# Optimization experiments

Measured on AMD Instinct MI355X. Metric: run time of the kernel, lower is better.

The kernel has to match this reference:

```python
import jax, jax.numpy as jnp
import numpy as np

B, N, M = 2, 4096, 4096
DQ = DKV = DOUT = 512
HEADS, DH = 8, 64
INNER = HEADS * DH
SCALE = DH ** -0.5


def _ln(x, g, b, eps=1e-5):
    mu = jnp.mean(x, axis=-1, keepdims=True)
    var = jnp.mean(jnp.square(x - mu), axis=-1, keepdims=True)
    return (x - mu) * jax.lax.rsqrt(var + eps) * g + b


def setup_inputs() -> dict:
    key = jax.random.key(0)
    ks = jax.random.split(key, 12)
    s = lambda fan: 1.0 / np.sqrt(fan)
    return {
        "q0": jax.random.normal(ks[0], (B, N, DQ), jnp.float32),
        "kv0": jax.random.normal(ks[1], (B, M, DKV), jnp.float32),
        "normq_g": jnp.ones((DQ,), jnp.float32),
        "normq_b": jnp.zeros((DQ,), jnp.float32),
        "normkv_g": jnp.ones((DKV,), jnp.float32),
        "normkv_b": jnp.zeros((DKV,), jnp.float32),
        "Wq": jax.random.normal(ks[2], (DQ, INNER), jnp.float32) * s(DQ),
        "Wk": jax.random.normal(ks[3], (DKV, INNER), jnp.float32) * s(DKV),
        "Wv": jax.random.normal(ks[4], (DKV, INNER), jnp.float32) * s(DKV),
        "Wr": jax.random.normal(ks[5], (INNER, DQ), jnp.float32) * s(INNER),
        "mlp_g": jnp.ones((DQ,), jnp.float32),
        "mlp_b": jnp.zeros((DQ,), jnp.float32),
        "W1": jax.random.normal(ks[6], (DQ, DOUT), jnp.float32) * s(DQ),
        "b1": jnp.zeros((DOUT,), jnp.float32),
        "W2": jax.random.normal(ks[7], (DOUT, DOUT), jnp.float32) * s(DOUT),
        "b2": jnp.zeros((DOUT,), jnp.float32),
    }


def reference(q0, kv0, normq_g, normq_b, normkv_g, normkv_b,
              Wq, Wk, Wv, Wr, mlp_g, mlp_b, W1, b1, W2, b2):
    # projections
    q = _ln(q0, normq_g, normq_b) @ Wq                    # [B,N,INNER]
    kv = _ln(kv0, normkv_g, normkv_b)                     # [B,M,DKV]
    k = kv @ Wk                                           # [B,M,INNER]
    v = kv @ Wv                                           # [B,M,INNER]
    # split heads: b n (h d) -> b h n d
    q = q.reshape(B, N, HEADS, DH).transpose(0, 2, 1, 3)
    k = k.reshape(B, M, HEADS, DH).transpose(0, 2, 1, 3)
    v = v.reshape(B, M, HEADS, DH).transpose(0, 2, 1, 3)
    dots = jnp.einsum('bhnd,bhmd->bhnm', q, k) * SCALE    # [B,H,N,M]
    attn = jax.nn.softmax(dots, axis=-1)
    out = jnp.einsum('bhnm,bhmd->bhnd', attn, v)          # [B,H,N,DH]
    out = out.transpose(0, 2, 1, 3).reshape(B, N, INNER)  # b h n d -> b n (h d)
    out = out @ Wr + q0                                   # [B,N,DQ]
    # MLP branch with residual
    h = _ln(out, mlp_g, mlp_b)
    h = jax.nn.relu(h @ W1 + b1) @ W2 + b2
    return out + h
```

## Files before the change

### kernel.cpp

```cpp
#include <hip/hip_runtime.h>

typedef unsigned short u16;
typedef unsigned int u32;
typedef __bf16 bf16x8 __attribute__((ext_vector_type(8)));
typedef float f32x4 __attribute__((ext_vector_type(4)));
typedef u16 u16x8 __attribute__((ext_vector_type(8)));

#define SC2 0.18033688011112042f

__device__ __forceinline__ u16 bf16rne(float f) {
  u32 u = __float_as_uint(f);
  u32 r = (u + 0x7FFFu + ((u >> 16) & 1u)) >> 16;
  return (u16)r;
}
__device__ __forceinline__ u32 packrne(float a, float b) {
  return (u32)bf16rne(a) | ((u32)bf16rne(b) << 16);
}
__device__ __forceinline__ float b2f(u16 v) {
  return __uint_as_float(((u32)v) << 16);
}

__device__ __forceinline__ void async16(const void* g, void* l) {
  __builtin_amdgcn_global_load_lds(
      (__attribute__((address_space(1))) void*)(g),
      (__attribute__((address_space(3))) void*)(l), 16, 0, 0);
}
template <int N>
__device__ __forceinline__ void vm_wait() {
  asm volatile("s_waitcnt vmcnt(%0)" ::"n"(N) : "memory");
}
__device__ __forceinline__ void lgkm_wait0() {
  asm volatile("s_waitcnt lgkmcnt(0)" ::: "memory");
}
__device__ __forceinline__ void bar() {
  asm volatile("s_barrier" ::: "memory");
}

__device__ __forceinline__ void ln_row(const float* xr, const float* gp,
                                       const float* bp, u16* orow, int lane) {
  const float* xl = xr + lane * 8;
  float4 a0 = *(const float4*)xl;
  float4 a1 = *(const float4*)(xl + 4);
  float v[8] = {a0.x, a0.y, a0.z, a0.w, a1.x, a1.y, a1.z, a1.w};
  float s = 0.f, s2 = 0.f;
#pragma unroll
  for (int j = 0; j < 8; ++j) { s += v[j]; s2 += v[j] * v[j]; }
#pragma unroll
  for (int off = 32; off; off >>= 1) {
    s += __shfl_xor(s, off);
    s2 += __shfl_xor(s2, off);
  }
  float mu = s * (1.0f / 512.0f);
  float rstd = rsqrtf(s2 * (1.0f / 512.0f) - mu * mu + 1e-5f);
  const float* gl = gp + lane * 8;
  const float* bl = bp + lane * 8;
  float4 g0 = *(const float4*)gl, g1 = *(const float4*)(gl + 4);
  float4 b0 = *(const float4*)bl, b1 = *(const float4*)(bl + 4);
  float gg[8] = {g0.x, g0.y, g0.z, g0.w, g1.x, g1.y, g1.z, g1.w};
  float bb[8] = {b0.x, b0.y, b0.z, b0.w, b1.x, b1.y, b1.z, b1.w};
  u16x8 ov;
#pragma unroll
  for (int j = 0; j < 8; ++j) ov[j] = bf16rne((v[j] - mu) * rstd * gg[j] + bb[j]);
  *(u16x8*)(orow + lane * 8) = ov;
}

__device__ __forceinline__ void lnb_row(const u16* xr, const float* gp,
                                        const float* bp, u16* orow, int lane) {
  u16x8 xv = *(const u16x8*)(xr + lane * 8);
  float v[8];
#pragma unroll
  for (int j = 0; j < 8; ++j) v[j] = b2f(xv[j]);
  float s = 0.f, s2 = 0.f;
#pragma unroll
  for (int j = 0; j < 8; ++j) { s += v[j]; s2 += v[j] * v[j]; }
#pragma unroll
  for (int off = 32; off; off >>= 1) {
    s += __shfl_xor(s, off);
    s2 += __shfl_xor(s2, off);
  }
  float mu = s * (1.0f / 512.0f);
  float rstd = rsqrtf(s2 * (1.0f / 512.0f) - mu * mu + 1e-5f);
  const float* gl = gp + lane * 8;
  const float* bl = bp + lane * 8;
  float4 g0 = *(const float4*)gl, g1 = *(const float4*)(gl + 4);
  float4 b0 = *(const float4*)bl, b1 = *(const float4*)(bl + 4);
  float gg[8] = {g0.x, g0.y, g0.z, g0.w, g1.x, g1.y, g1.z, g1.w};
  float bb[8] = {b0.x, b0.y, b0.z, b0.w, b1.x, b1.y, b1.z, b1.w};
  u16x8 ov;
#pragma unroll
  for (int j = 0; j < 8; ++j) ov[j] = bf16rne((v[j] - mu) * rstd * gg[j] + bb[j]);
  *(u16x8*)(orow + lane * 8) = ov;
}

__global__ __launch_bounds__(256) void prep_kernel(
    const float* __restrict__ w0, const float* __restrict__ w1,
    const float* __restrict__ w2, const float* __restrict__ w3,
    const float* __restrict__ w4, const float* __restrict__ w5,
    u16* __restrict__ wout,
    const float* __restrict__ x0, const float* __restrict__ g0,
    const float* __restrict__ b0, u16* __restrict__ o0,
    const float* __restrict__ x1, const float* __restrict__ g1,
    const float* __restrict__ b1, u16* __restrict__ o1) {
  __shared__ u16 T[64 * 72];
  int t = threadIdx.x;
  int bx = blockIdx.x;
  if (bx < 384) {
    int widx = bx >> 6, tile = bx & 63;
    int k0 = (tile & 7) * 64, n0 = (tile >> 3) * 64;
    const float* W = w0;
    if (widx == 1) W = w1; else if (widx == 2) W = w2; else if (widx == 3) W = w3;
    else if (widx == 4) W = w4; else if (widx == 5) W = w5;
#pragma unroll
    for (int p = 0; p < 4; ++p) {
      int kr = p * 16 + (t >> 4);
      int nc = (t & 15) * 4;
      float4 v = *(const float4*)(W + (size_t)(k0 + kr) * 512 + n0 + nc);
      T[(nc + 0) * 72 + kr] = bf16rne(v.x);
      T[(nc + 1) * 72 + kr] = bf16rne(v.y);
      T[(nc + 2) * 72 + kr] = bf16rne(v.z);
      T[(nc + 3) * 72 + kr] = bf16rne(v.w);
    }
    __syncthreads();
    u16* ob = wout + (size_t)widx * 262144;
#pragma unroll
    for (int p = 0; p < 2; ++p) {
      int idx = p * 256 + t;
      int nr = idx >> 3, ch = idx & 7;
      uint4 val = *(const uint4*)(T + nr * 72 + ch * 8);
      *(uint4*)(ob + (size_t)(n0 + nr) * 512 + k0 + ch * 8) = val;
    }
  } else {
    int w = t >> 6, lane = t & 63;
    size_t row = (size_t)(bx - 384) * 4 + w;
    if (row < 8192) {
      ln_row(x0 + row * 512, g0, b0, o0 + row * 512, lane);
    } else {
      size_t r2 = row - 8192;
      ln_row(x1 + r2 * 512, g1, b1, o1 + r2 * 512, lane);
    }
  }
}

__global__ __launch_bounds__(256) void lnb_kernel(
    const u16* __restrict__ x, const float* __restrict__ g,
    const float* __restrict__ b, u16* __restrict__ o) {
  int w = threadIdx.x >> 6, lane = threadIdx.x & 63;
  size_t row = (size_t)blockIdx.x * 4 + w;
  lnb_row(x + row * 512, g, b, o + row * 512, lane);
}

#define GSTAGE(buf, k0)                                                          \
  {                                                                              \
    _Pragma("unroll") for (int i = 0; i < 2; ++i) {                              \
      int s = t + 256 * i;                                                       \
      int mts = s >> 6, L = s & 63;                                             \
      async16(A + (size_t)(row0 + mts * 16 + (L & 15)) * 512 + (k0) + (L >> 4) * 8, \
              (char*)As[buf] + s * 16);                                          \
    }                                                                            \
    {                                                                            \
      int s = t;                                                                 \
      int nts = s >> 6, L = s & 63;                                             \
      async16(Bt + (size_t)(col0 + nts * 16 + (L & 15)) * 512 + (k0) + (L >> 4) * 8, \
              (char*)Bs[buf] + s * 16);                                          \
    }                                                                            \
  }

#define GEMM_CORE                                                                \
  GSTAGE(0, 0);                                                                  \
  GSTAGE(1, 32);                                                                 \
  GSTAGE(2, 64);                                                                 \
  _Pragma("unroll") for (int kk = 0; kk < 16; ++kk) {                            \
    if (kk <= 13) vm_wait<6>();                                                  \
    else if (kk == 14) vm_wait<3>();                                             \
    else vm_wait<0>();                                                           \
    bar();                                                                       \
    if (kk < 13) GSTAGE((kk + 3) & 3, (kk + 3) * 32);                            \
    const u16* Ac = As[kk & 3];                                                  \
    const u16* Bc = Bs[kk & 3];                                                  \
    bf16x8 Af[2], Bf[4];                                                         \
    _Pragma("unroll") for (int mt = 0; mt < 2; ++mt)                             \
        Af[mt] = *(const bf16x8*)(Ac + ((w * 2 + mt) * 64 + lane) * 8);          \
    _Pragma("unroll") for (int nt = 0; nt < 4; ++nt)                             \
        Bf[nt] = *(const bf16x8*)(Bc + (nt * 64 + lane) * 8);                    \
    _Pragma("unroll") for (int mt = 0; mt < 2; ++mt)                             \
        _Pragma("unroll") for (int nt = 0; nt < 4; ++nt)                         \
            acc[mt][nt] = __builtin_amdgcn_mfma_f32_16x16x32_bf16(               \
                Af[mt], Bf[nt], acc[mt][nt], 0, 0, 0);                           \
  }

template <int MODE>
__global__ __launch_bounds__(256) void gemm512_kernel(
    const u16* __restrict__ A, const u16* __restrict__ Bt, void* __restrict__ Cv,
    const float* __restrict__ bias, const float* __restrict__ res) {
  __shared__ __align__(16) u16 As[4][4096];
  __shared__ __align__(16) u16 Bs[4][2048];
  const int t = threadIdx.x;
  const int lane = t & 63;
  const int w = t >> 6;
  const int row0 = blockIdx.x * 128;
  const int col0 = blockIdx.y * 64;
  f32x4 acc[2][4];
#pragma unroll
  for (int i = 0; i < 2; ++i)
#pragma unroll
    for (int j = 0; j < 4; ++j) acc[i][j] = (f32x4){0.f, 0.f, 0.f, 0.f};

  GEMM_CORE

  const int q = lane >> 4, cl = lane & 15;
#pragma unroll
  for (int mt = 0; mt < 2; ++mt) {
#pragma unroll
    for (int nt = 0; nt < 4; ++nt) {
      int col = col0 + nt * 16 + cl;
#pragma unroll
      for (int r = 0; r < 4; ++r) {
        int row = row0 + (w * 2 + mt) * 16 + q * 4 + r;
        float v = acc[mt][nt][r];
        size_t idx = (size_t)row * 512 + col;
        if (MODE == 2) {
          v += bias[col];
          ((u16*)Cv)[idx] = bf16rne(fmaxf(v, 0.f));
        } else if (MODE == 3) {
          ((float*)Cv)[idx] = v + bias[col] + b2f(((const u16*)res)[idx]);
        } else if (MODE == 7) {
          ((u16*)Cv)[idx] = bf16rne(v + res[idx]);
        }
      }
    }
  }
}

__global__ __launch_bounds__(256) void proj_kernel(
    const u16* __restrict__ Aq, const u16* __restrict__ BtQ, u16* __restrict__ Qp,
    const u16* __restrict__ Akv, const u16* __restrict__ BtKV,
    u16* __restrict__ Kp, u16* __restrict__ VTp) {
  __shared__ __align__(16) u16 As[4][4096];
  __shared__ __align__(16) u16 Bs[4][2048];
  const int t = threadIdx.x;
  const int lane = t & 63;
  const int w = t >> 6;
  const int by = blockIdx.y;
  const bool isq = by < 8;
  const u16* A = isq ? Aq : Akv;
  const u16* Bt = isq ? BtQ : BtKV;
  const int row0 = blockIdx.x * 128;
  const int col0 = (isq ? by : by - 8) * 64;
  f32x4 acc[2][4];
#pragma unroll
  for (int i = 0; i < 2; ++i)
#pragma unroll
    for (int j = 0; j < 4; ++j) acc[i][j] = (f32x4){0.f, 0.f, 0.f, 0.f};

  GEMM_CORE

  const int q = lane >> 4, cl = lane & 15;
#pragma unroll
  for (int mt = 0; mt < 2; ++mt) {
#pragma unroll
    for (int nt = 0; nt < 4; ++nt) {
      int col = col0 + nt * 16 + cl;
      if (!isq && col >= 512) {
        int d = col - 512;
        int bb = row0 >> 12;
        int mloc = (row0 & 4095) + (w * 2 + mt) * 16 + q * 4;
        uint2 pk;
        pk.x = packrne(acc[mt][nt][0], acc[mt][nt][1]);
        pk.y = packrne(acc[mt][nt][2], acc[mt][nt][3]);
        *(uint2*)(VTp + ((size_t)bb * 512 + d) * 4096 + mloc) = pk;
        continue;
      }
#pragma unroll
      for (int r = 0; r < 4; ++r) {
        int row = row0 + (w * 2 + mt) * 16 + q * 4 + r;
        float v = acc[mt][nt][r];
        if (isq) {
          Qp[(size_t)row * 512 + col] = bf16rne(v * SC2);
        } else {
          Kp[(size_t)row * 512 + col] = bf16rne(v);
        }
      }
    }
  }
}

__global__ __launch_bounds__(128, 2) void attn_kernel(
    const u16* __restrict__ Q, const u16* __restrict__ K,
    const u16* __restrict__ VT, u16* __restrict__ O0, u16* __restrict__ O1,
    float* __restrict__ lpart) {
  __shared__ __align__(16) u16 Ks[2][4096];
  __shared__ __align__(16) u16 Vs[2][4096];
  __shared__ __align__(16) u16 Ps[2][1024];
  const int t = threadIdx.x;
  const int lane = t & 63;
  const int w = t >> 6;
  const int g = lane >> 4, cl = lane & 15;
  const int h = blockIdx.x, qt = blockIdx.y;
  const int b = blockIdx.z >> 1, sp = blockIdx.z & 1;
  const u16* Qg = Q + ((size_t)(b * 4096 + qt * 128 + w * 64)) * 512 + h * 64;
  const u16* Kg = K + ((size_t)(b * 4096 + sp * 2048)) * 512 + h * 64;
  const u16* VTg = VT + ((size_t)(b * 512 + h * 64)) * 4096 + sp * 2048;
  u16* Ob = (sp ? O1 : O0) + (((size_t)(b * 8 + h) * 4096) + qt * 128 + w * 64) * 64;
  float* lb = lpart + ((size_t)((sp * 2 + b) * 8 + h)) * 4096 + qt * 128 + w * 64;
  char* Pw = (char*)Ps[w];

#pragma unroll
  for (int i = 0; i < 8; ++i) {
    async16(Qg + (size_t)((i >> 1) * 16 + cl) * 512 + (i & 1) * 32 + g * 8,
            (char*)Ks[w] + (i * 64 + lane) * 16);
  }
  vm_wait<0>();
  bf16x8 Qb[4][2];
#pragma unroll
  for (int nt = 0; nt < 4; ++nt)
#pragma unroll
    for (int ks = 0; ks < 2; ++ks)
      Qb[nt][ks] = *(const bf16x8*)((char*)Ks[w] + ((nt * 2 + ks) * 64 + lane) * 16);
  lgkm_wait0();
  bar();

#define STAGEKV(buf, m0)                                                          \
  {                                                                               \
    _Pragma("unroll") for (int i = 0; i < 4; ++i) {                               \
      int s = t + 128 * i; int c = s >> 6; int L = s & 63;                        \
      async16(Kg + (size_t)((m0) + (c >> 1) * 16 + (L & 15)) * 512 + (c & 1) * 32 + (L >> 4) * 8, \
              (char*)Ks[buf] + s * 16);                                           \
    }                                                                             \
    _Pragma("unroll") for (int i = 0; i < 4; ++i) {                               \
      int s = t + 128 * i; int c = s >> 6; int L = s & 63;                        \
      async16(VTg + (size_t)((c >> 1) * 16 + (L & 15)) * 4096 + (m0) + (c & 1) * 32 + (L >> 4) * 8, \
              (char*)Vs[buf] + s * 16);                                           \
    }                                                                             \
  }

  STAGEKV(0, 0);

  u16x8 ou;
#pragma unroll
  for (int j = 0; j < 8; ++j) ou[j] = 0x3F80;
  bf16x8 ones = __builtin_bit_cast(bf16x8, ou);

  f32x4 Oa[4][4], ls[4];
#pragma unroll
  for (int i = 0; i < 4; ++i) {
    ls[i] = (f32x4){0.f, 0.f, 0.f, 0.f};
#pragma unroll
    for (int j = 0; j < 4; ++j) Oa[i][j] = (f32x4){0.f, 0.f, 0.f, 0.f};
  }
  const int s7 = cl & 7;

  for (int it = 0; it < 32; ++it) {
    if (it < 31) {
      STAGEKV((it + 1) & 1, (it + 1) * 64);
      vm_wait<8>();
    } else {
      vm_wait<0>();
    }
    bar();
    const u16* Kc = Ks[it & 1];
    const u16* Vc = Vs[it & 1];
    bf16x8 Kf[4][2], Vf[4][2];
#pragma unroll
    for (int mt = 0; mt < 4; ++mt)
#pragma unroll
      for (int ks = 0; ks < 2; ++ks) {
        Kf[mt][ks] = *(const bf16x8*)((const char*)Kc + ((mt * 2 + ks) * 64 + lane) * 16);
        Vf[mt][ks] = *(const bf16x8*)((const char*)Vc + ((mt * 2 + ks) * 64 + lane) * 16);
      }

#pragma unroll
    for (int nt = 0; nt < 4; ++nt) {
      f32x4 St[4];
#pragma unroll
      for (int mt = 0; mt < 4; ++mt) St[mt] = (f32x4){0.f, 0.f, 0.f, 0.f};
#pragma unroll
      for (int ks = 0; ks < 2; ++ks)
#pragma unroll
        for (int mt = 0; mt < 4; ++mt)
          St[mt] = __builtin_amdgcn_mfma_f32_16x16x32_bf16(Kf[mt][ks], Qb[nt][ks], St[mt], 0, 0, 0);

#pragma unroll
      for (int mt = 0; mt < 4; ++mt) {
        float p0 = __builtin_amdgcn_exp2f(St[mt][0]);
        float p1 = __builtin_amdgcn_exp2f(St[mt][1]);
        float p2 = __builtin_amdgcn_exp2f(St[mt][2]);
        float p3 = __builtin_amdgcn_exp2f(St[mt][3]);
        uint2 pk;
        pk.x = __builtin_amdgcn_perm(__float_as_uint(p1), __float_as_uint(p0), 0x07060302u);
        pk.y = __builtin_amdgcn_perm(__float_as_uint(p3), __float_as_uint(p2), 0x07060302u);
        *(uint2*)(Pw + cl * 128 + (((mt * 2 + (g >> 1)) ^ s7) << 4) + ((g & 1) << 3)) = pk;
      }
      bf16x8 Pb[2];
#pragma unroll
      for (int ks = 0; ks < 2; ++ks)
        Pb[ks] = *(const bf16x8*)(Pw + cl * 128 + (((ks * 4 + g) ^ s7) << 4));
      ls[nt] = __builtin_amdgcn_mfma_f32_16x16x32_bf16(ones, Pb[0], ls[nt], 0, 0, 0);
      ls[nt] = __builtin_amdgcn_mfma_f32_16x16x32_bf16(ones, Pb[1], ls[nt], 0, 0, 0);
#pragma unroll
      for (int ks = 0; ks < 2; ++ks)
#pragma unroll
        for (int mtd = 0; mtd < 4; ++mtd)
          Oa[mtd][nt] = __builtin_amdgcn_mfma_f32_16x16x32_bf16(Vf[mtd][ks], Pb[ks], Oa[mtd][nt], 0, 0, 0);
    }
    bar();
  }

#pragma unroll
  for (int nt = 0; nt < 4; ++nt) {
    int q = nt * 16 + cl;
#pragma unroll
    for (int mtd = 0; mtd < 4; ++mtd) {
      uint2 pk;
      pk.x = packrne(Oa[mtd][nt][0], Oa[mtd][nt][1]);
      pk.y = packrne(Oa[mtd][nt][2], Oa[mtd][nt][3]);
      *(uint2*)(Ob + (size_t)q * 64 + mtd * 16 + g * 4) = pk;
    }
    if (g == 0) lb[q] = ls[nt][0];
  }
}

__global__ __launch_bounds__(256) void combine_kernel(
    const u16* __restrict__ O0, const u16* __restrict__ O1,
    const float* __restrict__ lp, u16* __restrict__ out) {
  int idx = blockIdx.x * 256 + threadIdx.x;
  int dc = idx & 7;
  int q = (idx >> 3) & 4095;
  int h = (idx >> 15) & 7;
  int b = idx >> 18;
  size_t po = (((size_t)(b * 8 + h) * 4096) + q) * 64 + dc * 8;
  u16x8 a = *(const u16x8*)(O0 + po);
  u16x8 c = *(const u16x8*)(O1 + po);
  float l0 = lp[((size_t)(b * 8 + h)) * 4096 + q];
  float l1 = lp[((size_t)(16 + b * 8 + h)) * 4096 + q];
  float inv = 1.0f / (l0 + l1);
  u16x8 o;
#pragma unroll
  for (int j = 0; j < 8; ++j) o[j] = bf16rne((b2f(a[j]) + b2f(c[j])) * inv);
  *(u16x8*)(out + ((size_t)(b * 4096 + q)) * 512 + h * 64 + dc * 8) = o;
}

extern "C" void kernel_launch(void* const* d_in, const int* in_sizes, int n_in,
                              void* d_out, int out_size, void* d_ws, size_t ws_size,
                              hipStream_t stream) {
  const float* q0 = (const float*)d_in[0];
  const float* kv0 = (const float*)d_in[1];
  const float* nq_g = (const float*)d_in[2];
  const float* nq_b = (const float*)d_in[3];
  const float* nkv_g = (const float*)d_in[4];
  const float* nkv_b = (const float*)d_in[5];
  const float* Wq = (const float*)d_in[6];
  const float* Wk = (const float*)d_in[7];
  const float* Wv = (const float*)d_in[8];
  const float* Wr = (const float*)d_in[9];
  const float* mlp_g = (const float*)d_in[10];
  const float* mlp_b = (const float*)d_in[11];
  const float* W1 = (const float*)d_in[12];
  const float* b1 = (const float*)d_in[13];
  const float* W2 = (const float*)d_in[14];
  const float* b2 = (const float*)d_in[15];
  float* out = (float*)d_out;

  char* ws = (char*)d_ws;
  u16* obb = (u16*)(ws + 0);
  u16* O1p = (u16*)(ws + 0);
  u16* Qp = (u16*)(ws + 16777216);
  u16* aout = (u16*)(ws + 16777216);
  u16* Kp = (u16*)(ws + 25165824);
  u16* h1 = (u16*)(ws + 25165824);
  u16* VTp = (u16*)(ws + 33554432);
  u16* kvn2 = (u16*)(ws + 33554432);
  u16* wb = (u16*)(ws + 41943040);
  float* lpart = (float*)(ws + 45088768);
  u16* qn = (u16*)(ws + 46137344);
  u16* O0p = (u16*)(ws + 46137344);
  u16* kvn = (u16*)(ws + 54525952);
  u16* wqT = wb;
  u16* wkT = wb + 262144;
  u16* wrT = wb + 786432;
  u16* w1T = wb + 1048576;
  u16* w2T = wb + 1310720;

  dim3 blk(256);
  prep_kernel<<<4480, blk, 0, stream>>>(Wq, Wk, Wv, Wr, W1, W2, wb,
                                        q0, nq_g, nq_b, qn, kv0, nkv_g, nkv_b, kvn);
  proj_kernel<<<dim3(64, 24), blk, 0, stream>>>(qn, wqT, Qp, kvn, wkT, Kp, VTp);
  attn_kernel<<<dim3(8, 32, 4), dim3(128), 0, stream>>>(Qp, Kp, VTp, O0p, O1p, lpart);
  combine_kernel<<<2048, blk, 0, stream>>>(O0p, O1p, lpart, aout);
  gemm512_kernel<7><<<dim3(64, 8), blk, 0, stream>>>(aout, wrT, obb, nullptr, q0);
  lnb_kernel<<<2048, blk, 0, stream>>>(obb, mlp_g, mlp_b, kvn2);
  gemm512_kernel<2><<<dim3(64, 8), blk, 0, stream>>>(kvn2, w1T, h1, b1, nullptr);
  gemm512_kernel<3><<<dim3(64, 8), blk, 0, stream>>>(h1, w2T, out, b2, (const float*)obb);
}
```

Measured before the change: 286.4 us.

## Halve GEMM row tiles and split attention keys four ways for more blocks

All 512-wide GEMMs and the projection kernel now use 64-row tiles, so their grids have twice as many blocks. The attention kernel splits the key dimension into four chunks instead of two and processes 32-key tiles with smaller LDS buffers. It also raises its occupancy hint to 3 blocks per SM. The combine kernel now sums four partial outputs and four partial row sums. The aim is to fill the MI355X's many CUs better. The cost is more partial-output traffic, a heavier combine pass, and less data reuse per tile.

```diff
diff --git a/kernel.cpp b/kernel.cpp
--- a/kernel.cpp
+++ b/kernel.cpp
@@ -149,83 +149,71 @@
   lnb_row(x + row * 512, g, b, o + row * 512, lane);
 }
 
-#define GSTAGE(buf, k0)                                                          \
+#define GSTAGE64(buf, k0)                                                        \
   {                                                                              \
-    _Pragma("unroll") for (int i = 0; i < 2; ++i) {                              \
-      int s = t + 256 * i;                                                       \
-      int mts = s >> 6, L = s & 63;                                             \
-      async16(A + (size_t)(row0 + mts * 16 + (L & 15)) * 512 + (k0) + (L >> 4) * 8, \
-              (char*)As[buf] + s * 16);                                          \
+    {                                                                            \
+      int c = t >> 6, L = t & 63;                                                \
+      async16(A + (size_t)(row0 + c * 16 + (L & 15)) * 512 + (k0) + (L >> 4) * 8,\
+              (char*)As[buf] + t * 16);                                          \
+      async16(Bt + (size_t)(col0 + c * 16 + (L & 15)) * 512 + (k0) + (L >> 4) * 8,\
+              (char*)Bs[buf] + t * 16);                                          \
     }                                                                            \
-    {                                                                            \
-      int s = t;                                                                 \
-      int nts = s >> 6, L = s & 63;                                             \
-      async16(Bt + (size_t)(col0 + nts * 16 + (L & 15)) * 512 + (k0) + (L >> 4) * 8, \
-              (char*)Bs[buf] + s * 16);                                          \
-    }                                                                            \
-  }
-
-#define GEMM_CORE                                                                \
-  GSTAGE(0, 0);                                                                  \
-  GSTAGE(1, 32);                                                                 \
-  GSTAGE(2, 64);                                                                 \
+  }
+
+#define GEMM64_CORE                                                              \
+  GSTAGE64(0, 0);                                                                \
+  GSTAGE64(1, 32);                                                               \
+  GSTAGE64(2, 64);                                                               \
   _Pragma("unroll") for (int kk = 0; kk < 16; ++kk) {                            \
-    if (kk <= 13) vm_wait<6>();                                                  \
-    else if (kk == 14) vm_wait<3>();                                             \
+    if (kk <= 13) vm_wait<4>();                                                  \
+    else if (kk == 14) vm_wait<2>();                                             \
     else vm_wait<0>();                                                           \
     bar();                                                                       \
-    if (kk < 13) GSTAGE((kk + 3) & 3, (kk + 3) * 32);                            \
+    if (kk < 13) GSTAGE64((kk + 3) & 3, (kk + 3) * 32);                          \
     const u16* Ac = As[kk & 3];                                                  \
     const u16* Bc = Bs[kk & 3];                                                  \
-    bf16x8 Af[2], Bf[4];                                                         \
-    _Pragma("unroll") for (int mt = 0; mt < 2; ++mt)                             \
-        Af[mt] = *(const bf16x8*)(Ac + ((w * 2 + mt) * 64 + lane) * 8);          \
+    bf16x8 Af = *(const bf16x8*)(Ac + (w * 64 + lane) * 8);                      \
+    bf16x8 Bf[4];                                                                \
     _Pragma("unroll") for (int nt = 0; nt < 4; ++nt)                             \
         Bf[nt] = *(const bf16x8*)(Bc + (nt * 64 + lane) * 8);                    \
-    _Pragma("unroll") for (int mt = 0; mt < 2; ++mt)                             \
-        _Pragma("unroll") for (int nt = 0; nt < 4; ++nt)                         \
-            acc[mt][nt] = __builtin_amdgcn_mfma_f32_16x16x32_bf16(               \
-                Af[mt], Bf[nt], acc[mt][nt], 0, 0, 0);                           \
+    _Pragma("unroll") for (int nt = 0; nt < 4; ++nt)                             \
+        acc[nt] = __builtin_amdgcn_mfma_f32_16x16x32_bf16(Af, Bf[nt], acc[nt],   \
+                                                          0, 0, 0);              \
   }
 
 template <int MODE>
 __global__ __launch_bounds__(256) void gemm512_kernel(
     const u16* __restrict__ A, const u16* __restrict__ Bt, void* __restrict__ Cv,
     const float* __restrict__ bias, const float* __restrict__ res) {
-  __shared__ __align__(16) u16 As[4][4096];
+  __shared__ __align__(16) u16 As[4][2048];
   __shared__ __align__(16) u16 Bs[4][2048];
   const int t = threadIdx.x;
   const int lane = t & 63;
   const int w = t >> 6;
-  const int row0 = blockIdx.x * 128;
+  const int row0 = blockIdx.x * 64;
   const int col0 = blockIdx.y * 64;
-  f32x4 acc[2][4];
-#pragma unroll
-  for (int i = 0; i < 2; ++i)
-#pragma unroll
-    for (int j = 0; j < 4; ++j) acc[i][j] = (f32x4){0.f, 0.f, 0.f, 0.f};
-
-  GEMM_CORE
-
-  const int q = lane >> 4, cl = lane & 15;
-#pragma unroll
-  for (int mt = 0; mt < 2; ++mt) {
-#pragma unroll
-    for (int nt = 0; nt < 4; ++nt) {
-      int col = col0 + nt * 16 + cl;
-#pragma unroll
-      for (int r = 0; r < 4; ++r) {
-        int row = row0 + (w * 2 + mt) * 16 + q * 4 + r;
-        float v = acc[mt][nt][r];
-        size_t idx = (size_t)row * 512 + col;
-        if (MODE == 2) {
-          v += bias[col];
-          ((u16*)Cv)[idx] = bf16rne(fmaxf(v, 0.f));
-        } else if (MODE == 3) {
-          ((float*)Cv)[idx] = v + bias[col] + b2f(((const u16*)res)[idx]);
-        } else if (MODE == 7) {
-          ((u16*)Cv)[idx] = bf16rne(v + res[idx]);
-        }
+  f32x4 acc[4];
+#pragma unroll
+  for (int j = 0; j < 4; ++j) acc[j] = (f32x4){0.f, 0.f, 0.f, 0.f};
+
+  GEMM64_CORE
+
+  const int g = lane >> 4, cl = lane & 15;
+#pragma unroll
+  for (int nt = 0; nt < 4; ++nt) {
+    int col = col0 + nt * 16 + cl;
+#pragma unroll
+    for (int r = 0; r < 4; ++r) {
+      int row = row0 + w * 16 + g * 4 + r;
+      float v = acc[nt][r];
+      size_t idx = (size_t)row * 512 + col;
+      if (MODE == 2) {
+        v += bias[col];
+        ((u16*)Cv)[idx] = bf16rne(fmaxf(v, 0.f));
+      } else if (MODE == 3) {
+        ((float*)Cv)[idx] = v + bias[col] + b2f(((const u16*)res)[idx]);
+      } else if (MODE == 7) {
+        ((u16*)Cv)[idx] = bf16rne(v + res[idx]);
       }
     }
   }
@@ -235,7 +223,7 @@
     const u16* __restrict__ Aq, const u16* __restrict__ BtQ, u16* __restrict__ Qp,
     const u16* __restrict__ Akv, const u16* __restrict__ BtKV,
     u16* __restrict__ Kp, u16* __restrict__ VTp) {
-  __shared__ __align__(16) u16 As[4][4096];
+  __shared__ __align__(16) u16 As[4][2048];
   __shared__ __align__(16) u16 Bs[4][2048];
   const int t = threadIdx.x;
   const int lane = t & 63;
@@ -244,70 +232,67 @@
   const bool isq = by < 8;
   const u16* A = isq ? Aq : Akv;
   const u16* Bt = isq ? BtQ : BtKV;
-  const int row0 = blockIdx.x * 128;
+  const int row0 = blockIdx.x * 64;
   const int col0 = (isq ? by : by - 8) * 64;
-  f32x4 acc[2][4];
-#pragma unroll
-  for (int i = 0; i < 2; ++i)
-#pragma unroll
-    for (int j = 0; j < 4; ++j) acc[i][j] = (f32x4){0.f, 0.f, 0.f, 0.f};
-
-  GEMM_CORE
-
-  const int q = lane >> 4, cl = lane & 15;
-#pragma unroll
-  for (int mt = 0; mt < 2; ++mt) {
-#pragma unroll
-    for (int nt = 0; nt < 4; ++nt) {
-      int col = col0 + nt * 16 + cl;
-      if (!isq && col >= 512) {
-        int d = col - 512;
-        int bb = row0 >> 12;
-        int mloc = (row0 & 4095) + (w * 2 + mt) * 16 + q * 4;
-        uint2 pk;
-        pk.x = packrne(acc[mt][nt][0], acc[mt][nt][1]);
-        pk.y = packrne(acc[mt][nt][2], acc[mt][nt][3]);
-        *(uint2*)(VTp + ((size_t)bb * 512 + d) * 4096 + mloc) = pk;
-        continue;
+  f32x4 acc[4];
+#pragma unroll
+  for (int j = 0; j < 4; ++j) acc[j] = (f32x4){0.f, 0.f, 0.f, 0.f};
+
+  GEMM64_CORE
+
+  const int g = lane >> 4, cl = lane & 15;
+#pragma unroll
+  for (int nt = 0; nt < 4; ++nt) {
+    int col = col0 + nt * 16 + cl;
+    if (!isq && col >= 512) {
+      int d = col - 512;
+      int bb = row0 >> 12;
+      int mloc = (row0 & 4095) + w * 16 + g * 4;
+      uint2 pk;
+      pk.x = packrne(acc[nt][0], acc[nt][1]);
+      pk.y = packrne(acc[nt][2], acc[nt][3]);
+      *(uint2*)(VTp + ((size_t)bb * 512 + d) * 4096 + mloc) = pk;
+      continue;
+    }
+#pragma unroll
+    for (int r = 0; r < 4; ++r) {
+      int row = row0 + w * 16 + g * 4 + r;
+      float v = acc[nt][r];
+      if (isq) {
+        Qp[(size_t)row * 512 + col] = bf16rne(v * SC2);
+      } else {
+        Kp[(size_t)row * 512 + col] = bf16rne(v);
       }
-#pragma unroll
-      for (int r = 0; r < 4; ++r) {
-        int row = row0 + (w * 2 + mt) * 16 + q * 4 + r;
-        float v = acc[mt][nt][r];
-        if (isq) {
-          Qp[(size_t)row * 512 + col] = bf16rne(v * SC2);
-        } else {
-          Kp[(size_t)row * 512 + col] = bf16rne(v);
-        }
-      }
-    }
-  }
-}
-
-__global__ __launch_bounds__(128, 2) void attn_kernel(
+    }
+  }
+}
+
+__global__ __launch_bounds__(128, 3) void attn_kernel(
     const u16* __restrict__ Q, const u16* __restrict__ K,
     const u16* __restrict__ VT, u16* __restrict__ O0, u16* __restrict__ O1,
-    float* __restrict__ lpart) {
-  __shared__ __align__(16) u16 Ks[2][4096];
-  __shared__ __align__(16) u16 Vs[2][4096];
-  __shared__ __align__(16) u16 Ps[2][1024];
+    u16* __restrict__ O2, u16* __restrict__ O3, float* __restrict__ lpart) {
+  __shared__ __align__(16) u16 Ks[2][2048];
+  __shared__ __align__(16) u16 Vs[2][2048];
+  __shared__ __align__(16) u16 Ps[2][512];
   const int t = threadIdx.x;
   const int lane = t & 63;
   const int w = t >> 6;
   const int g = lane >> 4, cl = lane & 15;
   const int h = blockIdx.x, qt = blockIdx.y;
-  const int b = blockIdx.z >> 1, sp = blockIdx.z & 1;
+  const int b = blockIdx.z >> 2, sp = blockIdx.z & 3;
   const u16* Qg = Q + ((size_t)(b * 4096 + qt * 128 + w * 64)) * 512 + h * 64;
-  const u16* Kg = K + ((size_t)(b * 4096 + sp * 2048)) * 512 + h * 64;
-  const u16* VTg = VT + ((size_t)(b * 512 + h * 64)) * 4096 + sp * 2048;
-  u16* Ob = (sp ? O1 : O0) + (((size_t)(b * 8 + h) * 4096) + qt * 128 + w * 64) * 64;
+  const u16* Kg = K + ((size_t)(b * 4096 + sp * 1024)) * 512 + h * 64;
+  const u16* VTg = VT + ((size_t)(b * 512 + h * 64)) * 4096 + sp * 1024;
+  u16* Op = (sp == 0) ? O0 : (sp == 1) ? O1 : (sp == 2) ? O2 : O3;
+  u16* Ob = Op + (((size_t)(b * 8 + h) * 4096) + qt * 128 + w * 64) * 64;
   float* lb = lpart + ((size_t)((sp * 2 + b) * 8 + h)) * 4096 + qt * 128 + w * 64;
   char* Pw = (char*)Ps[w];
+  char* Qscr = w ? (char*)Vs : (char*)Ks;
 
 #pragma unroll
   for (int i = 0; i < 8; ++i) {
     async16(Qg + (size_t)((i >> 1) * 16 + cl) * 512 + (i & 1) * 32 + g * 8,
-            (char*)Ks[w] + (i * 64 + lane) * 16);
+            Qscr + (i * 64 + lane) * 16);
   }
   vm_wait<0>();
   bf16x8 Qb[4][2];
@@ -315,20 +300,20 @@
   for (int nt = 0; nt < 4; ++nt)
 #pragma unroll
     for (int ks = 0; ks < 2; ++ks)
-      Qb[nt][ks] = *(const bf16x8*)((char*)Ks[w] + ((nt * 2 + ks) * 64 + lane) * 16);
+      Qb[nt][ks] = *(const bf16x8*)(Qscr + ((nt * 2 + ks) * 64 + lane) * 16);
   lgkm_wait0();
   bar();
 
 #define STAGEKV(buf, m0)                                                          \
   {                                                                               \
-    _Pragma("unroll") for (int i = 0; i < 4; ++i) {                               \
+    _Pragma("unroll") for (int i = 0; i < 2; ++i) {                               \
       int s = t + 128 * i; int c = s >> 6; int L = s & 63;                        \
       async16(Kg + (size_t)((m0) + (c >> 1) * 16 + (L & 15)) * 512 + (c & 1) * 32 + (L >> 4) * 8, \
               (char*)Ks[buf] + s * 16);                                           \
     }                                                                             \
-    _Pragma("unroll") for (int i = 0; i < 4; ++i) {                               \
+    _Pragma("unroll") for (int i = 0; i < 2; ++i) {                               \
       int s = t + 128 * i; int c = s >> 6; int L = s & 63;                        \
-      async16(VTg + (size_t)((c >> 1) * 16 + (L & 15)) * 4096 + (m0) + (c & 1) * 32 + (L >> 4) * 8, \
+      async16(VTg + (size_t)(c * 16 + (L & 15)) * 4096 + (m0) + (L >> 4) * 8,     \
               (char*)Vs[buf] + s * 16);                                           \
     }                                                                             \
   }
@@ -347,40 +332,41 @@
 #pragma unroll
     for (int j = 0; j < 4; ++j) Oa[i][j] = (f32x4){0.f, 0.f, 0.f, 0.f};
   }
-  const int s7 = cl & 7;
+  const int s3 = cl & 3;
 
   for (int it = 0; it < 32; ++it) {
     if (it < 31) {
-      STAGEKV((it + 1) & 1, (it + 1) * 64);
-      vm_wait<8>();
+      STAGEKV((it + 1) & 1, (it + 1) * 32);
+      vm_wait<4>();
     } else {
       vm_wait<0>();
     }
     bar();
     const u16* Kc = Ks[it & 1];
     const u16* Vc = Vs[it & 1];
-    bf16x8 Kf[4][2], Vf[4][2];
-#pragma unroll
-    for (int mt = 0; mt < 4; ++mt)
-#pragma unroll
-      for (int ks = 0; ks < 2; ++ks) {
+    bf16x8 Kf[2][2], Vf[4];
+#pragma unroll
+    for (int mt = 0; mt < 2; ++mt)
+#pragma unroll
+      for (int ks = 0; ks < 2; ++ks)
         Kf[mt][ks] = *(const bf16x8*)((const char*)Kc + ((mt * 2 + ks) * 64 + lane) * 16);
-        Vf[mt][ks] = *(const bf16x8*)((const char*)Vc + ((mt * 2 + ks) * 64 + lane) * 16);
-      }
+#pragma unroll
+    for (int mtd = 0; mtd < 4; ++mtd)
+      Vf[mtd] = *(const bf16x8*)((const char*)Vc + ((mtd * 64 + lane)) * 16);
 
 #pragma unroll
     for (int nt = 0; nt < 4; ++nt) {
-      f32x4 St[4];
-#pragma unroll
-      for (int mt = 0; mt < 4; ++mt) St[mt] = (f32x4){0.f, 0.f, 0.f, 0.f};
+      f32x4 St[2];
+#pragma unroll
+      for (int mt = 0; mt < 2; ++mt) St[mt] = (f32x4){0.f, 0.f, 0.f, 0.f};
 #pragma unroll
       for (int ks = 0; ks < 2; ++ks)
 #pragma unroll
-        for (int mt = 0; mt < 4; ++mt)
+        for (int mt = 0; mt < 2; ++mt)
           St[mt] = __builtin_amdgcn_mfma_f32_16x16x32_bf16(Kf[mt][ks], Qb[nt][ks], St[mt], 0, 0, 0);
 
 #pragma unroll
-      for (int mt = 0; mt < 4; ++mt) {
+      for (int mt = 0; mt < 2; ++mt) {
         float p0 = __builtin_amdgcn_exp2f(St[mt][0]);
         float p1 = __builtin_amdgcn_exp2f(St[mt][1]);
         float p2 = __builtin_amdgcn_exp2f(St[mt][2]);
@@ -388,19 +374,13 @@
         uint2 pk;
         pk.x = __builtin_amdgcn_perm(__float_as_uint(p1), __float_as_uint(p0), 0x07060302u);
         pk.y = __builtin_amdgcn_perm(__float_as_uint(p3), __float_as_uint(p2), 0x07060302u);
-        *(uint2*)(Pw + cl * 128 + (((mt * 2 + (g >> 1)) ^ s7) << 4) + ((g & 1) << 3)) = pk;
+        *(uint2*)(Pw + cl * 64 + (((mt * 2 + (g >> 1)) ^ s3) << 4) + ((g & 1) << 3)) = pk;
       }
-      bf16x8 Pb[2];
-#pragma unroll
-      for (int ks = 0; ks < 2; ++ks)
-        Pb[ks] = *(const bf16x8*)(Pw + cl * 128 + (((ks * 4 + g) ^ s7) << 4));
-      ls[nt] = __builtin_amdgcn_mfma_f32_16x16x32_bf16(ones, Pb[0], ls[nt], 0, 0, 0);
-      ls[nt] = __builtin_amdgcn_mfma_f32_16x16x32_bf16(ones, Pb[1], ls[nt], 0, 0, 0);
-#pragma unroll
-      for (int ks = 0; ks < 2; ++ks)
-#pragma unroll
-        for (int mtd = 0; mtd < 4; ++mtd)
-          Oa[mtd][nt] = __builtin_amdgcn_mfma_f32_16x16x32_bf16(Vf[mtd][ks], Pb[ks], Oa[mtd][nt], 0, 0, 0);
+      bf16x8 Pb = *(const bf16x8*)(Pw + cl * 64 + ((g ^ s3) << 4));
+      ls[nt] = __builtin_amdgcn_mfma_f32_16x16x32_bf16(ones, Pb, ls[nt], 0, 0, 0);
+#pragma unroll
+      for (int mtd = 0; mtd < 4; ++mtd)
+        Oa[mtd][nt] = __builtin_amdgcn_mfma_f32_16x16x32_bf16(Vf[mtd], Pb, Oa[mtd][nt], 0, 0, 0);
     }
     bar();
   }
@@ -421,6 +401,7 @@
 
 __global__ __launch_bounds__(256) void combine_kernel(
     const u16* __restrict__ O0, const u16* __restrict__ O1,
+    const u16* __restrict__ O2, const u16* __restrict__ O3,
     const float* __restrict__ lp, u16* __restrict__ out) {
   int idx = blockIdx.x * 256 + threadIdx.x;
   int dc = idx & 7;
@@ -428,14 +409,17 @@
   int h = (idx >> 15) & 7;
   int b = idx >> 18;
   size_t po = (((size_t)(b * 8 + h) * 4096) + q) * 64 + dc * 8;
-  u16x8 a = *(const u16x8*)(O0 + po);
-  u16x8 c = *(const u16x8*)(O1 + po);
-  float l0 = lp[((size_t)(b * 8 + h)) * 4096 + q];
-  float l1 = lp[((size_t)(16 + b * 8 + h)) * 4096 + q];
-  float inv = 1.0f / (l0 + l1);
+  u16x8 a0 = *(const u16x8*)(O0 + po);
+  u16x8 a1 = *(const u16x8*)(O1 + po);
+  u16x8 a2 = *(const u16x8*)(O2 + po);
+  u16x8 a3 = *(const u16x8*)(O3 + po);
+  size_t lo = ((size_t)(b * 8 + h)) * 4096 + q;
+  float l = lp[lo] + lp[lo + 65536] + lp[lo + 131072] + lp[lo + 196608];
+  float inv = 1.0f / l;
   u16x8 o;
 #pragma unroll
-  for (int j = 0; j < 8; ++j) o[j] = bf16rne((b2f(a[j]) + b2f(c[j])) * inv);
+  for (int j = 0; j < 8; ++j)
+    o[j] = bf16rne((b2f(a0[j]) + b2f(a1[j]) + b2f(a2[j]) + b2f(a3[j])) * inv);
   *(u16x8*)(out + ((size_t)(b * 4096 + q)) * 512 + h * 64 + dc * 8) = o;
 }
 
@@ -462,7 +446,8 @@
 
   char* ws = (char*)d_ws;
   u16* obb = (u16*)(ws + 0);
-  u16* O1p = (u16*)(ws + 0);
+  u16* O2p = (u16*)(ws + 0);
+  u16* O3p = (u16*)(ws + 8388608);
   u16* Qp = (u16*)(ws + 16777216);
   u16* aout = (u16*)(ws + 16777216);
   u16* Kp = (u16*)(ws + 25165824);
@@ -474,6 +459,7 @@
   u16* qn = (u16*)(ws + 46137344);
   u16* O0p = (u16*)(ws + 46137344);
   u16* kvn = (u16*)(ws + 54525952);
+  u16* O1p = (u16*)(ws + 54525952);
   u16* wqT = wb;
   u16* wkT = wb + 262144;
   u16* wrT = wb + 786432;
@@ -483,11 +469,12 @@
   dim3 blk(256);
   prep_kernel<<<4480, blk, 0, stream>>>(Wq, Wk, Wv, Wr, W1, W2, wb,
                                         q0, nq_g, nq_b, qn, kv0, nkv_g, nkv_b, kvn);
-  proj_kernel<<<dim3(64, 24), blk, 0, stream>>>(qn, wqT, Qp, kvn, wkT, Kp, VTp);
-  attn_kernel<<<dim3(8, 32, 4), dim3(128), 0, stream>>>(Qp, Kp, VTp, O0p, O1p, lpart);
-  combine_kernel<<<2048, blk, 0, stream>>>(O0p, O1p, lpart, aout);
-  gemm512_kernel<7><<<dim3(64, 8), blk, 0, stream>>>(aout, wrT, obb, nullptr, q0);
+  proj_kernel<<<dim3(128, 24), blk, 0, stream>>>(qn, wqT, Qp, kvn, wkT, Kp, VTp);
+  attn_kernel<<<dim3(8, 32, 8), dim3(128), 0, stream>>>(Qp, Kp, VTp, O0p, O1p,
+                                                        O2p, O3p, lpart);
+  combine_kernel<<<2048, blk, 0, stream>>>(O0p, O1p, O2p, O3p, lpart, aout);
+  gemm512_kernel<7><<<dim3(128, 8), blk, 0, stream>>>(aout, wrT, obb, nullptr, q0);
   lnb_kernel<<<2048, blk, 0, stream>>>(obb, mlp_g, mlp_b, kvn2);
-  gemm512_kernel<2><<<dim3(64, 8), blk, 0, stream>>>(kvn2, w1T, h1, b1, nullptr);
-  gemm512_kernel<3><<<dim3(64, 8), blk, 0, stream>>>(h1, w2T, out, b2, (const float*)obb);
-}
+  gemm512_kernel<2><<<dim3(128, 8), blk, 0, stream>>>(kvn2, w1T, h1, b1, nullptr);
+  gemm512_kernel<3><<<dim3(128, 8), blk, 0, stream>>>(h1, w2T, out, b2, (const float*)obb);
+}
```

Result: slower. 349.2 us (+21.9%).
